# Optimization experiments

Measured on AMD Instinct MI355X. Metric: run time of the kernel, lower is better.

Reference implementation:

```python
import jax, jax.numpy as jnp
import numpy as np

B, D, N = 2, 512, 2048
H, MQ, MV = 8, 64, 64
SCALE = 1.0 / np.sqrt(D).astype(np.float32)  # 1/sqrt(num_dim_q), full dim


def setup_inputs() -> dict:
    key = jax.random.key(0)
    ks = jax.random.split(key, 9)
    s = 0.02
    return {
        "Q": jax.random.normal(ks[0], (B, D, N), jnp.float32),
        "Wq": jax.random.normal(ks[1], (MQ * H, D), jnp.float32) * s,
        "bq": jnp.zeros((MQ * H,), jnp.float32),
        "Wk": jax.random.normal(ks[2], (MQ * H, D), jnp.float32) * s,
        "bk": jnp.zeros((MQ * H,), jnp.float32),
        "Wv": jax.random.normal(ks[3], (MV * H, D), jnp.float32) * s,
        "bv": jnp.zeros((MV * H,), jnp.float32),
        "Wo": jax.random.normal(ks[4], (D, MV * H), jnp.float32) * s,
        "bo": jnp.zeros((D,), jnp.float32),
    }


def _conv1x1(x, W, b):
    # Conv1d with kernel_size=1 == per-position linear: [B,Cin,N] -> [B,Cout,N]
    return jnp.einsum("bcn,oc->bon", x, W) + b[None, :, None]


def reference(Q, Wq, bq, Wk, bk, Wv, bv, Wo, bo):
    q = _conv1x1(Q, Wq, bq)  # [B, MQ*H, N]
    k = _conv1x1(Q, Wk, bk)
    v = _conv1x1(Q, Wv, bv)  # [B, MV*H, N]
    b = Q.shape[0]
    n = Q.shape[2]
    # channel index factors as (dim, head): channel = d*H + h (matches torch .view)
    q = q.reshape(b, MQ, H, n)
    k = k.reshape(b, MQ, H, n)
    v = v.reshape(b, MV, H, n)
    scores = jnp.einsum("bdhq,bdhk->bhqk", q, k) * SCALE  # [B,H,Nq,Nk]
    attn = jax.nn.softmax(scores, axis=-1)
    o = jnp.einsum("bhqk,bdhk->bdhq", attn, v)  # [B, MV, H, Nq]
    o = o.reshape(b, MV * H, n)
    return _conv1x1(o, Wo, bo)  # [B, D, N]
```

## Files before the change

kernel.cpp:

```cpp
#include <hip/hip_runtime.h>

#define DEV __device__ __forceinline__

typedef __bf16 bf16;
typedef __bf16 bf16x8 __attribute__((ext_vector_type(8)));
typedef __bf16 bf16x4 __attribute__((ext_vector_type(4)));
typedef float f32x4 __attribute__((ext_vector_type(4)));
typedef float f32x16 __attribute__((ext_vector_type(16)));
typedef unsigned int u32x4 __attribute__((ext_vector_type(4)));

#define SCALE_F (0.04419417382415922f * 1.4426950408889634f)

DEV void gload_lds16(const void* g, void* l) {
  __builtin_amdgcn_global_load_lds(
      (const __attribute__((address_space(1))) void*)g,
      (__attribute__((address_space(3))) void*)l, 16, 0, 0);
}

DEV f32x4 mfma16(bf16x8 a, bf16x8 b, f32x4 c) {
  return __builtin_amdgcn_mfma_f32_16x16x32_bf16(a, b, c, 0, 0, 0);
}
DEV f32x16 mfma32(bf16x8 a, bf16x8 b, f32x16 c) {
  return __builtin_amdgcn_mfma_f32_32x32x16_bf16(a, b, c, 0, 0, 0);
}

DEV unsigned int pkbf(float a, float b) {
  unsigned short ua = __builtin_bit_cast(unsigned short, (bf16)a);
  unsigned short ub = __builtin_bit_cast(unsigned short, (bf16)b);
  return (unsigned int)ua | ((unsigned int)ub << 16);
}

__global__ __launch_bounds__(256) void prep(
    const float* __restrict__ Q,
    const float* __restrict__ Wq, const float* __restrict__ bq,
    const float* __restrict__ Wk, const float* __restrict__ bk,
    const float* __restrict__ Wv, const float* __restrict__ bv,
    const float* __restrict__ Wo,
    bf16* __restrict__ Wf, float* __restrict__ biasf, bf16* __restrict__ Wor,
    bf16* __restrict__ Qt) {
  __shared__ float tile[64][65];
  int bid = blockIdx.x;
  int t = threadIdx.x;
  if (bid < 2048) {
    int row = bid;
    if (row < 1536) {
      const float* src;
      float scale = 1.0f;
      if (row < 512)       { src = Wq + (size_t)row * 512; scale = SCALE_F; }
      else if (row < 1024) { src = Wk + (size_t)(row - 512) * 512; }
      else                 { src = Wv + (size_t)(row - 1024) * 512; }
      for (int c = t; c < 512; c += 256)
        Wf[(size_t)row * 512 + c] = (bf16)(src[c] * scale);
      if (t == 0) {
        float bb;
        if (row < 512)       bb = bq[row] * SCALE_F;
        else if (row < 1024) bb = bk[row - 512];
        else                 bb = bv[row - 1024];
        biasf[row] = bb;
      }
    } else {
      int r = row - 1536;
      for (int c2 = t; c2 < 512; c2 += 256) {
        int hh = c2 >> 6, dd = c2 & 63;
        Wor[(size_t)r * 512 + c2] = (bf16)Wo[(size_t)r * 512 + dd * 8 + hh];
      }
    }
  } else {
    int id2 = bid - 2048;
    int n0 = (id2 & 31) * 64;
    int d0 = ((id2 >> 5) & 7) * 64;
    int b = id2 >> 8;
    int r = t >> 2, cw = t & 3;
    const float* src = Q + ((size_t)(b * 512 + d0 + r)) * 2048 + n0 + cw * 16;
#pragma unroll
    for (int e4 = 0; e4 < 4; ++e4) {
      float4 v = *(const float4*)(src + e4 * 4);
      tile[r][cw * 16 + e4 * 4 + 0] = v.x;
      tile[r][cw * 16 + e4 * 4 + 1] = v.y;
      tile[r][cw * 16 + e4 * 4 + 2] = v.z;
      tile[r][cw * 16 + e4 * 4 + 3] = v.w;
    }
    __syncthreads();
    bf16x8 o0{}, o1{};
#pragma unroll
    for (int e = 0; e < 8; ++e) {
      o0[e] = (bf16)tile[cw * 16 + e][r];
      o1[e] = (bf16)tile[cw * 16 + 8 + e][r];
    }
    bf16* dst = Qt + ((size_t)(b * 2048 + n0 + r)) * 512 + d0 + cw * 16;
    *(bf16x8*)dst = o0;
    *((bf16x8*)dst + 1) = o1;
  }
}

__global__ __launch_bounds__(256) void qkv_gemm(
    const bf16* __restrict__ Wf, const bf16* __restrict__ Qt,
    const float* __restrict__ biasf,
    bf16* __restrict__ qp, bf16* __restrict__ kp, bf16* __restrict__ vn) {
  __shared__ bf16 Al[128 * 32];
  __shared__ bf16 Bl[64 * 32];
  int b = blockIdx.z;
  int c0 = blockIdx.x * 128;
  int p0 = blockIdx.y * 64;
  int tid = threadIdx.x, w = tid >> 6, lane = tid & 63;
  int wm = w >> 1, wn = w & 1;
  int g = lane >> 4, l15 = lane & 15;

  const bf16* Abase = Wf + (size_t)c0 * 512;
  const bf16* Bbase = Qt + ((size_t)b * 2048 + p0) * 512;

  f32x4 acc[4][2] = {};

  for (int ks = 0; ks < 16; ++ks) {
    int k0 = ks * 32;
    __syncthreads();
#pragma unroll
    for (int i = 0; i < 2; ++i) {
      int rowl = w * 32 + i * 16 + (lane >> 2);
      gload_lds16(Abase + (size_t)rowl * 512 + k0 + (lane & 3) * 8,
                  Al + (w * 32 + i * 16) * 32);
    }
    {
      int browl = w * 16 + (lane >> 2);
      gload_lds16(Bbase + (size_t)browl * 512 + k0 + (lane & 3) * 8,
                  Bl + w * 16 * 32);
    }
    __syncthreads();
    bf16x8 a[4], bb[2];
#pragma unroll
    for (int mi = 0; mi < 4; ++mi)
      a[mi] = *(const bf16x8*)(Al + (wm * 64 + mi * 16 + l15) * 32 + g * 8);
#pragma unroll
    for (int ni = 0; ni < 2; ++ni)
      bb[ni] = *(const bf16x8*)(Bl + (wn * 32 + ni * 16 + l15) * 32 + g * 8);
#pragma unroll
    for (int mi = 0; mi < 4; ++mi)
#pragma unroll
      for (int ni = 0; ni < 2; ++ni)
        acc[mi][ni] = mfma16(a[mi], bb[ni], acc[mi][ni]);
  }

#pragma unroll
  for (int mi = 0; mi < 4; ++mi) {
#pragma unroll
    for (int ni = 0; ni < 2; ++ni) {
#pragma unroll
      for (int r = 0; r < 4; ++r) {
        int row = c0 + wm * 64 + mi * 16 + g * 4 + r;
        int p = p0 + wn * 32 + ni * 16 + l15;
        float val = acc[mi][ni][r] + biasf[row];
        bf16 hv = (bf16)val;
        if (row < 512) {
          int c = row;
          qp[(((size_t)b * 8 + (c & 7)) * 2048 + p) * 64 + (c >> 3)] = hv;
        } else if (row < 1024) {
          int c = row - 512;
          kp[(((size_t)b * 8 + (c & 7)) * 2048 + p) * 64 + (c >> 3)] = hv;
        } else {
          int c = row - 1024;
          vn[((size_t)b * 512 + c) * 2048 + p] = hv;
        }
      }
    }
  }
}

__global__ __launch_bounds__(512, 4) void attn_k(
    const bf16* __restrict__ qp, const bf16* __restrict__ kp,
    const bf16* __restrict__ vn, bf16* __restrict__ Op,
    float* __restrict__ mbuf, float* __restrict__ lbuf, int TS) {
  __shared__ bf16 Ks[2][64 * 64];
  __shared__ bf16 Vs[2][64 * 64];
  int q0 = blockIdx.x * 256;
  int bh = blockIdx.y;
  int z = blockIdx.z;
  int b = bh >> 3, h = bh & 7;
  int tid = threadIdx.x, w = tid >> 6, lane = tid & 63;
  int l31 = lane & 31, hi = lane >> 5;

  bf16x8 qreg[4];
#pragma unroll
  for (int kd = 0; kd < 4; ++kd)
    qreg[kd] = *(const bf16x8*)(
        qp + ((size_t)bh * 2048 + q0 + w * 32 + l31) * 64 + kd * 16 + hi * 8);

  int krow = tid >> 3;
  int kch = (tid & 7) ^ (krow & 7);

  const bf16* Kall = kp + (size_t)bh * 2048 * 64 + (size_t)z * TS * 4096;
  const bf16* Vall = vn + ((size_t)(b * 512 + h)) * 2048 + (size_t)z * TS * 64;

  gload_lds16(Kall + (size_t)krow * 64 + kch * 8, Ks[0] + w * 512);
  gload_lds16(Vall + (size_t)krow * 16384 + kch * 8, Vs[0] + w * 512);

  f32x16 oacc0 = {}, oacc1 = {};
  float mrow = -1e30f, rs = 0.0f;

  __syncthreads();

  for (int t = 0; t < TS; ++t) {
    int cur = t & 1, nxt = cur ^ 1;
    int tn = (t < TS - 1) ? t + 1 : t;

    gload_lds16(Kall + (size_t)tn * 4096 + (size_t)krow * 64 + kch * 8,
                Ks[nxt] + w * 512);
    gload_lds16(Vall + (size_t)tn * 64 + (size_t)krow * 16384 + kch * 8,
                Vs[nxt] + w * 512);

    f32x16 st0 = {}, st1 = {};
    __builtin_amdgcn_s_setprio(1);
#pragma unroll
    for (int kd = 0; kd < 4; ++kd) {
      int sw = ((kd * 2 + hi) ^ (l31 & 7)) << 3;
      bf16x8 kb0 = *(const bf16x8*)(Ks[cur] + l31 * 64 + sw);
      bf16x8 kb1 = *(const bf16x8*)(Ks[cur] + (32 + l31) * 64 + sw);
      st0 = mfma32(kb0, qreg[kd], st0);
      st1 = mfma32(kb1, qreg[kd], st1);
    }
    __builtin_amdgcn_s_setprio(0);

    float rm = st0[0];
#pragma unroll
    for (int r = 1; r < 16; ++r) rm = fmaxf(rm, st0[r]);
#pragma unroll
    for (int r = 0; r < 16; ++r) rm = fmaxf(rm, st1[r]);
    rm = fmaxf(rm, __shfl_xor(rm, 32));

    if (__any(rm > mrow + 8.0f)) {
      float nm = fmaxf(mrow, rm);
      float esc = __builtin_amdgcn_exp2f(mrow - nm);
      mrow = nm;
      rs *= esc;
#pragma unroll
      for (int r = 0; r < 16; ++r) {
        int ql = (r & 3) + 8 * (r >> 2) + 4 * hi;
        float er = __shfl(esc, ql, 64);
        oacc0[r] *= er;
        oacc1[r] *= er;
      }
    }

    bf16x8 pa[4];
#pragma unroll
    for (int tile = 0; tile < 2; ++tile) {
      float pv[16];
#pragma unroll
      for (int r = 0; r < 16; ++r) {
        float v = __builtin_amdgcn_exp2f((tile ? st1[r] : st0[r]) - mrow);
        pv[r] = v;
        rs += v;
      }
      unsigned int r0d0 = pkbf(pv[0], pv[1]),   r0d1 = pkbf(pv[2], pv[3]);
      unsigned int r1d0 = pkbf(pv[4], pv[5]),   r1d1 = pkbf(pv[6], pv[7]);
      unsigned int r2d0 = pkbf(pv[8], pv[9]),   r2d1 = pkbf(pv[10], pv[11]);
      unsigned int r3d0 = pkbf(pv[12], pv[13]), r3d1 = pkbf(pv[14], pv[15]);
      asm volatile("v_permlane32_swap_b32 %0, %1" : "+v"(r0d0), "+v"(r1d0));
      asm volatile("v_permlane32_swap_b32 %0, %1" : "+v"(r0d1), "+v"(r1d1));
      pa[tile * 2] = __builtin_bit_cast(bf16x8, (u32x4){r0d0, r0d1, r1d0, r1d1});
      asm volatile("v_permlane32_swap_b32 %0, %1" : "+v"(r2d0), "+v"(r3d0));
      asm volatile("v_permlane32_swap_b32 %0, %1" : "+v"(r2d1), "+v"(r3d1));
      pa[tile * 2 + 1] =
          __builtin_bit_cast(bf16x8, (u32x4){r2d0, r2d1, r3d0, r3d1});
    }

    __builtin_amdgcn_s_setprio(1);
#pragma unroll
    for (int kt = 0; kt < 4; ++kt) {
      int sw0 = ((kt * 2 + hi) ^ (l31 & 7)) << 3;
      bf16x8 vb0 = *(const bf16x8*)(Vs[cur] + l31 * 64 + sw0);
      bf16x8 vb1 = *(const bf16x8*)(Vs[cur] + (32 + l31) * 64 + sw0);
      oacc0 = mfma32(pa[kt], vb0, oacc0);
      oacc1 = mfma32(pa[kt], vb1, oacc1);
    }
    __builtin_amdgcn_s_setprio(0);

    __syncthreads();
  }

  rs += __shfl_xor(rs, 32);

  size_t zb = (size_t)(z * 16 + bh) * 2048 + q0 + w * 32;
#pragma unroll
  for (int r = 0; r < 16; ++r) {
    int ql = (r & 3) + 8 * (r >> 2) + 4 * hi;
    Op[(zb + ql) * 64 + l31] = (bf16)oacc0[r];
    Op[(zb + ql) * 64 + 32 + l31] = (bf16)oacc1[r];
  }
  if (hi == 0) {
    mbuf[zb + l31] = mrow;
    lbuf[zb + l31] = rs;
  }
}

__global__ __launch_bounds__(256) void combine(
    const bf16* __restrict__ Op, const float* __restrict__ mbuf,
    const float* __restrict__ lbuf, bf16* __restrict__ oh, int NS) {
  int idx = blockIdx.x * 256 + threadIdx.x;
  int row = idx >> 2;
  int dc = (idx & 3) * 16;

  float M = -1e30f;
  for (int z = 0; z < NS; ++z) M = fmaxf(M, mbuf[(size_t)z * 32768 + row]);

  float L = 0.0f;
  float acc[16];
#pragma unroll
  for (int e = 0; e < 16; ++e) acc[e] = 0.0f;

  for (int z = 0; z < NS; ++z) {
    float wz = __builtin_amdgcn_exp2f(mbuf[(size_t)z * 32768 + row] - M);
    L += wz * lbuf[(size_t)z * 32768 + row];
    const bf16x8* p = (const bf16x8*)(Op + ((size_t)z * 32768 + row) * 64 + dc);
#pragma unroll
    for (int v = 0; v < 2; ++v) {
      bf16x8 x = p[v];
#pragma unroll
      for (int e = 0; e < 8; ++e) acc[v * 8 + e] += wz * (float)x[e];
    }
  }
  float invL = 1.0f / L;
  bf16x8* po = (bf16x8*)(oh + (size_t)row * 64 + dc);
#pragma unroll
  for (int v = 0; v < 2; ++v) {
    bf16x8 o;
#pragma unroll
    for (int e = 0; e < 8; ++e) o[e] = (bf16)(acc[v * 8 + e] * invL);
    po[v] = o;
  }
}

__global__ __launch_bounds__(256) void out_gemm(
    const bf16* __restrict__ Wor, const bf16* __restrict__ oh,
    const float* __restrict__ bo, float* __restrict__ out) {
  __shared__ bf16 Al[128 * 32];
  __shared__ bf16 Bl[64 * 32];
  int b = blockIdx.z;
  int r0 = blockIdx.x * 128;
  int p0 = blockIdx.y * 64;
  int tid = threadIdx.x, w = tid >> 6, lane = tid & 63;
  int wm = w >> 1, wn = w & 1;
  int g = lane >> 4, l15 = lane & 15;

  const bf16* Abase = Wor + (size_t)r0 * 512;

  f32x4 acc[4][2] = {};

  for (int ks = 0; ks < 16; ++ks) {
    int k0 = ks * 32;
    int hh = k0 >> 6, d0 = k0 & 63;
    const bf16* Bbase = oh + (((size_t)b * 8 + hh) * 2048 + p0) * 64 + d0;
    __syncthreads();
#pragma unroll
    for (int i = 0; i < 2; ++i) {
      int rowl = w * 32 + i * 16 + (lane >> 2);
      gload_lds16(Abase + (size_t)rowl * 512 + k0 + (lane & 3) * 8,
                  Al + (w * 32 + i * 16) * 32);
    }
    {
      int browl = w * 16 + (lane >> 2);
      gload_lds16(Bbase + (size_t)browl * 64 + (lane & 3) * 8,
                  Bl + w * 16 * 32);
    }
    __syncthreads();
    bf16x8 a[4], bb[2];
#pragma unroll
    for (int mi = 0; mi < 4; ++mi)
      a[mi] = *(const bf16x8*)(Al + (wm * 64 + mi * 16 + l15) * 32 + g * 8);
#pragma unroll
    for (int ni = 0; ni < 2; ++ni)
      bb[ni] = *(const bf16x8*)(Bl + (wn * 32 + ni * 16 + l15) * 32 + g * 8);
#pragma unroll
    for (int mi = 0; mi < 4; ++mi)
#pragma unroll
      for (int ni = 0; ni < 2; ++ni)
        acc[mi][ni] = mfma16(a[mi], bb[ni], acc[mi][ni]);
  }

#pragma unroll
  for (int mi = 0; mi < 4; ++mi) {
#pragma unroll
    for (int ni = 0; ni < 2; ++ni) {
#pragma unroll
      for (int r = 0; r < 4; ++r) {
        int row = r0 + wm * 64 + mi * 16 + g * 4 + r;
        int p = p0 + wn * 32 + ni * 16 + l15;
        out[((size_t)b * 512 + row) * 2048 + p] = acc[mi][ni][r] + bo[row];
      }
    }
  }
}

extern "C" void kernel_launch(void* const* d_in, const int* in_sizes, int n_in,
                              void* d_out, int out_size, void* d_ws, size_t ws_size,
                              hipStream_t stream) {
  (void)in_sizes; (void)n_in; (void)out_size;
  const float* Q  = (const float*)d_in[0];
  const float* Wq = (const float*)d_in[1];
  const float* bq = (const float*)d_in[2];
  const float* Wk = (const float*)d_in[3];
  const float* bk = (const float*)d_in[4];
  const float* Wv = (const float*)d_in[5];
  const float* bv = (const float*)d_in[6];
  const float* Wo = (const float*)d_in[7];
  const float* bo = (const float*)d_in[8];
  float* out = (float*)d_out;

  char* ws = (char*)d_ws;
  bf16*  Wf    = (bf16*)(ws + 0);
  bf16*  Wor   = (bf16*)(ws + 1572864);
  float* biasf = (float*)(ws + 2097152);
  bf16*  Qt    = (bf16*)(ws + 2103296);
  bf16*  qp    = (bf16*)(ws + 6297600);
  bf16*  kp    = (bf16*)(ws + 10491904);
  bf16*  vn    = (bf16*)(ws + 14686208);

  size_t need4 = 18880512ull + 4ull * 4194304 + 2ull * 4ull * 131072;
  int NS = (ws_size >= need4) ? 4 : 2;
  int TS = 32 / NS;

  bf16*  Opart = (bf16*)(ws + 18880512);
  float* mbuf  = (float*)(ws + 18880512 + (size_t)NS * 4194304);
  float* lbuf  = (float*)(ws + 18880512 + (size_t)NS * 4194304 +
                          (size_t)NS * 131072);
  bf16*  oh    = Opart;

  prep<<<dim3(2560), dim3(256), 0, stream>>>(Q, Wq, bq, Wk, bk, Wv, bv, Wo,
                                             Wf, biasf, Wor, Qt);
  qkv_gemm<<<dim3(12, 32, 2), dim3(256), 0, stream>>>(Wf, Qt, biasf, qp, kp, vn);
  attn_k<<<dim3(8, 16, NS), dim3(512), 0, stream>>>(qp, kp, vn, Opart, mbuf,
                                                    lbuf, TS);
  combine<<<dim3(512), dim3(256), 0, stream>>>(Opart, mbuf, lbuf, oh, NS);
  out_gemm<<<dim3(4, 32, 2), dim3(256), 0, stream>>>(Wor, oh, bo, out);
}
```

Before: 80.43 us.

## Fuse split-K attention combine into output projection GEMM

Removes the separate combine kernel: the output GEMM now computes per-row softmax merge weights into shared memory and merges the NS partial attention outputs while loading its B tile. This saves a kernel launch and the write and re-read of the merged intermediate. In exchange, each of the 4 row-tile blocks recomputes the merge for the same B columns, so partial-output reads are repeated. The B tile load also becomes a synchronous register path instead of an async global-to-LDS load. The grid is flattened with a swizzled block index.

```diff
diff --git a/kernel.cpp b/kernel.cpp
--- a/kernel.cpp
+++ b/kernel.cpp
@@ -292,63 +292,57 @@
   }
 }
 
-__global__ __launch_bounds__(256) void combine(
-    const bf16* __restrict__ Op, const float* __restrict__ mbuf,
-    const float* __restrict__ lbuf, bf16* __restrict__ oh, int NS) {
-  int idx = blockIdx.x * 256 + threadIdx.x;
-  int row = idx >> 2;
-  int dc = (idx & 3) * 16;
-
-  float M = -1e30f;
-  for (int z = 0; z < NS; ++z) M = fmaxf(M, mbuf[(size_t)z * 32768 + row]);
-
-  float L = 0.0f;
-  float acc[16];
-#pragma unroll
-  for (int e = 0; e < 16; ++e) acc[e] = 0.0f;
-
-  for (int z = 0; z < NS; ++z) {
-    float wz = __builtin_amdgcn_exp2f(mbuf[(size_t)z * 32768 + row] - M);
-    L += wz * lbuf[(size_t)z * 32768 + row];
-    const bf16x8* p = (const bf16x8*)(Op + ((size_t)z * 32768 + row) * 64 + dc);
-#pragma unroll
-    for (int v = 0; v < 2; ++v) {
-      bf16x8 x = p[v];
-#pragma unroll
-      for (int e = 0; e < 8; ++e) acc[v * 8 + e] += wz * (float)x[e];
-    }
-  }
-  float invL = 1.0f / L;
-  bf16x8* po = (bf16x8*)(oh + (size_t)row * 64 + dc);
-#pragma unroll
-  for (int v = 0; v < 2; ++v) {
-    bf16x8 o;
-#pragma unroll
-    for (int e = 0; e < 8; ++e) o[e] = (bf16)(acc[v * 8 + e] * invL);
-    po[v] = o;
-  }
-}
-
-__global__ __launch_bounds__(256) void out_gemm(
-    const bf16* __restrict__ Wor, const bf16* __restrict__ oh,
-    const float* __restrict__ bo, float* __restrict__ out) {
+__global__ __launch_bounds__(256) void outc(
+    const bf16* __restrict__ Wor, const bf16* __restrict__ Op,
+    const float* __restrict__ mbuf, const float* __restrict__ lbuf,
+    const float* __restrict__ bo, float* __restrict__ out, int NS) {
   __shared__ bf16 Al[128 * 32];
   __shared__ bf16 Bl[64 * 32];
-  int b = blockIdx.z;
-  int r0 = blockIdx.x * 128;
-  int p0 = blockIdx.y * 64;
+  __shared__ float wls[512][4];
+
+  int bid = blockIdx.x;
+  int rx = (bid >> 3) & 3;
+  int yz = (bid & 7) + 8 * (bid >> 5);
+  int r0 = rx * 128;
+  int p0 = (yz & 31) * 64;
+  int b = yz >> 5;
+
   int tid = threadIdx.x, w = tid >> 6, lane = tid & 63;
   int wm = w >> 1, wn = w & 1;
   int g = lane >> 4, l15 = lane & 15;
 
+#pragma unroll
+  for (int it = 0; it < 2; ++it) {
+    int pr = tid + it * 256;
+    int hh = pr >> 6, pl = pr & 63;
+    size_t row = ((size_t)(b * 8 + hh)) * 2048 + p0 + pl;
+    float mz[4], lz[4];
+    float M = -1e30f;
+    for (int z = 0; z < NS; ++z) {
+      mz[z] = mbuf[(size_t)z * 32768 + row];
+      lz[z] = lbuf[(size_t)z * 32768 + row];
+      M = fmaxf(M, mz[z]);
+    }
+    float L = 0.0f;
+    for (int z = 0; z < NS; ++z) {
+      float wz = __builtin_amdgcn_exp2f(mz[z] - M);
+      mz[z] = wz;
+      L += wz * lz[z];
+    }
+    float invL = 1.0f / L;
+    for (int z = 0; z < NS; ++z) wls[pr][z] = mz[z] * invL;
+  }
+
   const bf16* Abase = Wor + (size_t)r0 * 512;
+
+  int browl = w * 16 + (lane >> 2);
+  int ch8 = (lane & 3) * 8;
 
   f32x4 acc[4][2] = {};
 
   for (int ks = 0; ks < 16; ++ks) {
     int k0 = ks * 32;
     int hh = k0 >> 6, d0 = k0 & 63;
-    const bf16* Bbase = oh + (((size_t)b * 8 + hh) * 2048 + p0) * 64 + d0;
     __syncthreads();
 #pragma unroll
     for (int i = 0; i < 2; ++i) {
@@ -357,9 +351,21 @@
                   Al + (w * 32 + i * 16) * 32);
     }
     {
-      int browl = w * 16 + (lane >> 2);
-      gload_lds16(Bbase + (size_t)browl * 64 + (lane & 3) * 8,
-                  Bl + w * 16 * 32);
+      size_t base = ((size_t)(b * 8 + hh)) * 2048 + p0 + browl;
+      float facc[8];
+#pragma unroll
+      for (int e = 0; e < 8; ++e) facc[e] = 0.0f;
+      for (int z = 0; z < NS; ++z) {
+        bf16x8 v = *(const bf16x8*)(Op + ((size_t)z * 32768 + base) * 64 +
+                                    d0 + ch8);
+        float wz = wls[(hh << 6) | browl][z];
+#pragma unroll
+        for (int e = 0; e < 8; ++e) facc[e] += wz * (float)v[e];
+      }
+      bf16x8 pk;
+#pragma unroll
+      for (int e = 0; e < 8; ++e) pk[e] = (bf16)facc[e];
+      *(bf16x8*)(Bl + browl * 32 + ch8) = pk;
     }
     __syncthreads();
     bf16x8 a[4], bb[2];
@@ -422,13 +428,11 @@
   float* mbuf  = (float*)(ws + 18880512 + (size_t)NS * 4194304);
   float* lbuf  = (float*)(ws + 18880512 + (size_t)NS * 4194304 +
                           (size_t)NS * 131072);
-  bf16*  oh    = Opart;
 
   prep<<<dim3(2560), dim3(256), 0, stream>>>(Q, Wq, bq, Wk, bk, Wv, bv, Wo,
                                              Wf, biasf, Wor, Qt);
   qkv_gemm<<<dim3(12, 32, 2), dim3(256), 0, stream>>>(Wf, Qt, biasf, qp, kp, vn);
   attn_k<<<dim3(8, 16, NS), dim3(512), 0, stream>>>(qp, kp, vn, Opart, mbuf,
                                                     lbuf, TS);
-  combine<<<dim3(512), dim3(256), 0, stream>>>(Opart, mbuf, lbuf, oh, NS);
-  out_gemm<<<dim3(4, 32, 2), dim3(256), 0, stream>>>(Wor, oh, bo, out);
-}
+  outc<<<dim3(256), dim3(256), 0, stream>>>(Wor, Opart, mbuf, lbuf, bo, out, NS);
+}
```

Result: slower. 84.89 us (+5.5%).
